# Kernel optimization log

Measured on AMD Instinct MI355X. Metric: run time of the kernel, lower is better.

The kernel has to match this reference:

```python
import jax, jax.numpy as jnp
import numpy as np

V, E, H, L, B, T = 20000, 128, 192, 3, 256, 512


def _lstm_dir(x, W_ih, W_hh, b, reverse):
    """One direction of one LSTM layer. x: [B,T,I] -> (outputs [B,T,H], final h [B,H]).
    PyTorch gate order: i, f, g, o. b = b_ih + b_hh (summed, same math)."""
    gx = jnp.einsum('bti,gi->tbg', x, W_ih) + b  # [T,B,4H] input contributions, precomputed
    Wh = W_hh.T                                   # [H,4H]

    def step(carry, g):
        h, c = carry
        z = g + h @ Wh                            # [B,4H]
        i, f, gg, o = jnp.split(z, 4, axis=-1)
        c = jax.nn.sigmoid(f) * c + jax.nn.sigmoid(i) * jnp.tanh(gg)
        h = jax.nn.sigmoid(o) * jnp.tanh(c)
        return (h, c), h

    h0 = jnp.zeros((x.shape[0], H), x.dtype)
    (hT, _), hs = jax.lax.scan(step, (h0, h0), gx, reverse=reverse)
    return hs.transpose(1, 0, 2), hT


def setup_inputs() -> dict:
    key = jax.random.key(0)
    ks = jax.random.split(key, 12)
    k = 1.0 / np.sqrt(H)
    u = lambda kk, shape: jax.random.uniform(kk, shape, jnp.float32, -k, k)
    emb = jax.random.normal(ks[0], (V, E), jnp.float32)
    emb = emb.at[0].set(0.0)  # padding_idx=0
    return {
        'x': jax.random.randint(ks[1], (B, T), 0, V),
        'emb': emb,
        'W_ih0': u(ks[2], (2, 4 * H, E)),        # layer 0, [dir, 4H, E]
        'W_hh0': u(ks[3], (2, 4 * H, H)),
        'b0': u(ks[4], (2, 4 * H)) + u(ks[5], (2, 4 * H)),  # b_ih + b_hh
        'W_ih_r': u(ks[6], (L - 1, 2, 4 * H, 2 * H)),       # layers 1..2 take concat(fwd,bwd)
        'W_hh_r': u(ks[7], (L - 1, 2, 4 * H, H)),
        'b_r': u(ks[8], (L - 1, 2, 4 * H)) + u(ks[9], (L - 1, 2, 4 * H)),
        'fc_w': u(ks[10], (1, 2 * H)),
        'fc_b': u(ks[11], (1,)),
    }


def reference(x, emb, W_ih0, W_hh0, b0, W_ih_r, W_hh_r, b_r, fc_w, fc_b):
    h = emb[x]  # [B,T,E]
    hT_f = hT_b = None
    for l in range(L):
        if l == 0:
            Wi, Wh, bb = W_ih0, W_hh0, b0
        else:
            Wi, Wh, bb = W_ih_r[l - 1], W_hh_r[l - 1], b_r[l - 1]
        out_f, hT_f = _lstm_dir(h, Wi[0], Wh[0], bb[0], reverse=False)
        out_b, hT_b = _lstm_dir(h, Wi[1], Wh[1], bb[1], reverse=True)
        h = jnp.concatenate([out_f, out_b], axis=-1)  # [B,T,2H]
        # inter-layer dropout is inactive at inference
    last = jnp.concatenate([hT_f, hT_b], axis=-1)     # [B,2H]  (hidden[-2], hidden[-1])
    return last @ fc_w.T + fc_b                        # [B,1]
```

## Files before the change

### kernel.cpp

```cpp
#include <hip/hip_runtime.h>
#include <hip/hip_bf16.h>


typedef _Float16 f16;
typedef unsigned int u32;
typedef _Float16 f16x8 __attribute__((ext_vector_type(8)));
typedef float f32x4 __attribute__((ext_vector_type(4)));

__device__ __forceinline__ float sigm(float x) {
  float e = __builtin_amdgcn_exp2f(x * -1.44269504088896f);
  return __builtin_amdgcn_rcpf(1.0f + e);
}
__device__ __forceinline__ float tanh_(float x) {
  float e = __builtin_amdgcn_exp2f(x * -2.88539008177793f);
  return __builtin_fmaf(2.0f, __builtin_amdgcn_rcpf(1.0f + e), -1.0f);
}


__global__ void castk(const float* __restrict__ s, f16* __restrict__ d, int n) {
  int i = blockIdx.x * 256 + threadIdx.x;
  int st = gridDim.x * 256;
  for (; i < n; i += st) d[i] = (f16)s[i];
}

__global__ void castwhh(const float* __restrict__ src, f16* __restrict__ dst) {
  int o = blockIdx.x * 256 + threadIdx.x;
  int e = o & 7, rest = o >> 3;
  int l = rest & 63; rest >>= 6;
  int kk = rest % 6; rest /= 6;
  int g = rest & 3; rest >>= 2;
  int w = rest % 12; int dir = rest / 12;
  int lo16 = l & 15, lhi = l >> 4;
  dst[o] = (f16)src[(size_t)(dir * 768 + g * 192 + w * 16 + lo16) * 192 + kk * 32 + lhi * 8 + e];
}

__global__ void embedk(const int* __restrict__ x, const float* __restrict__ emb,
                       f16* __restrict__ A0) {
  int row = blockIdx.x * 8 + (threadIdx.x >> 5);
  int t = row >> 8, b = row & 255;
  int xi = x[b * 512 + t];
  int c = (threadIdx.x & 31) * 4;
  float4 v = *(const float4*)(emb + (size_t)xi * 128 + c);
  union { f16 h[4]; uint2 u; } p;
  p.h[0] = (f16)v.x; p.h[1] = (f16)v.y; p.h[2] = (f16)v.z; p.h[3] = (f16)v.w;
  *(uint2*)(A0 + (size_t)row * 128 + c) = p.u;
}

template <int KD>
__global__ __launch_bounds__(768)
void fusedk(const f16* __restrict__ in, const f16* __restrict__ Bt,
            const float* __restrict__ bias,
            const u32* __restrict__ gxR, u32* __restrict__ gxW,
            const f16* __restrict__ whh16,
            f16* __restrict__ outh, float* __restrict__ hT,
            f16* __restrict__ carh, float* __restrict__ carc,
            int c, int cg, int NC, int TC, int doLstm, int wOut, int wHT) {
  union SMem {
    struct { uint4 A[512]; uint4 B[1536]; } g;
    f16 hb[2][16 * 200];
  };
  __shared__ __align__(16) SMem sm;
  const int wg = blockIdx.x;
  const int tid = threadIdx.x;
  const int l = tid & 63, w = tid >> 6;
  const int lo16 = l & 15, lhi = l >> 4;
  const int TCm1 = TC - 1;

  if (doLstm && wg < 32) {
    const int dir = wg & 1, bblk = wg >> 1;
    const int u0 = w * 16;
    const int bb = bblk * 16 + lhi * 4;
    const int dc = dir * 192;
    const int hb0 = lhi * 800 + u0 + lo16;

    f16x8 wf[4][6];
#pragma unroll
    for (int g = 0; g < 4; ++g)
#pragma unroll
      for (int kk = 0; kk < 6; ++kk)
        wf[g][kk] = *(const f16x8*)(whh16 + ((((size_t)dir * 12 + w) * 4 + g) * 6 + kk) * 512 + l * 8);

    float cq[4];
    if (c == 0) {
      f16* hz = (f16*)sm.hb;
      for (int i = tid; i < 2 * 16 * 200; i += 768) hz[i] = (f16)0.f;
#pragma unroll
      for (int q = 0; q < 4; ++q) cq[q] = 0.f;
    } else {
#pragma unroll
      for (int q = 0; q < 4; ++q) {
        size_t ci = ((size_t)dir * 256 + bb + q) * 192 + u0 + lo16;
        cq[q] = carc[ci];
        sm.hb[0][(lhi * 4 + q) * 200 + u0 + lo16] = carh[ci];
      }
    }
    __syncthreads();

    const int tb0 = dir ? (511 - c * TC) : (c * TC);
    f16* outp = outh + ((size_t)tb0 * 256 + bb) * 384 + dc + u0 + lo16;
    const ptrdiff_t ostep = dir ? -(ptrdiff_t)98304 : (ptrdiff_t)98304;

    u32 ga[8], gb[8];
    {
      const int tl0 = dir ? TCm1 : 0;
      size_t wb = ((((size_t)dir * TC + tl0) * 16 + bblk) * 12 + w) * 512;
#pragma unroll
      for (int k2 = 0; k2 < 8; ++k2) ga[k2] = gxR[wb + k2 * 64 + l];
    }

#define RSTEP(S, CUR, NXT)                                                         \
  do {                                                                             \
    {                                                                              \
      int snx = ((S) + 1 < TC) ? (S) + 1 : (S);                                    \
      int tln = dir ? (TCm1 - snx) : snx;                                          \
      size_t wb = ((((size_t)dir * TC + tln) * 16 + bblk) * 12 + w) * 512;         \
      _Pragma("unroll") for (int k2 = 0; k2 < 8; ++k2) NXT[k2] = gxR[wb + k2 * 64 + l]; \
    }                                                                              \
    f32x4 ac[4];                                                                   \
    _Pragma("unroll") for (int g_ = 0; g_ < 4; ++g_) {                             \
      union { u32 u; f16 h[2]; } p0, p1;                                           \
      p0.u = CUR[2 * g_]; p1.u = CUR[2 * g_ + 1];                                  \
      ac[g_][0] = (float)p0.h[0]; ac[g_][1] = (float)p0.h[1];                      \
      ac[g_][2] = (float)p1.h[0]; ac[g_][3] = (float)p1.h[1];                      \
    }                                                                              \
    {                                                                              \
      const f16* hcur = sm.hb[(S) & 1];                                            \
      _Pragma("unroll") for (int kk = 0; kk < 6; ++kk) {                           \
        f16x8 av = *(const f16x8*)(hcur + lo16 * 200 + kk * 32 + lhi * 8);         \
        ac[0] = __builtin_amdgcn_mfma_f32_16x16x32_f16(av, wf[0][kk], ac[0], 0, 0, 0); \
        ac[1] = __builtin_amdgcn_mfma_f32_16x16x32_f16(av, wf[1][kk], ac[1], 0, 0, 0); \
        ac[2] = __builtin_amdgcn_mfma_f32_16x16x32_f16(av, wf[2][kk], ac[2], 0, 0, 0); \
        ac[3] = __builtin_amdgcn_mfma_f32_16x16x32_f16(av, wf[3][kk], ac[3], 0, 0, 0); \
      }                                                                            \
    }                                                                              \
    f16* hnew = sm.hb[((S) + 1) & 1];                                              \
    _Pragma("unroll") for (int q = 0; q < 4; ++q) {                                \
      float iv = sigm(ac[0][q]), fv = sigm(ac[1][q]);                              \
      float gv = tanh_(ac[2][q]), ov = sigm(ac[3][q]);                             \
      cq[q] = fv * cq[q] + iv * gv;                                                \
      float hv = ov * tanh_(cq[q]);                                                \
      f16 hh = (f16)hv;                                                            \
      hnew[hb0 + q * 200] = hh;                                                    \
      if (wOut) outp[q * 384] = hh;                                                \
      if ((S) == TCm1) {                                                           \
        size_t ci = ((size_t)dir * 256 + bb + q) * 192 + u0 + lo16;                \
        carh[ci] = hh;                                                             \
        carc[ci] = cq[q];                                                          \
        if (wHT && c == NC - 1) hT[ci] = hv;                                       \
      }                                                                            \
    }                                                                              \
    outp += ostep;                                                                 \
    asm volatile("s_waitcnt lgkmcnt(0)" ::: "memory");                             \
    __builtin_amdgcn_s_barrier();                                                  \
    asm volatile("" ::: "memory");                                                 \
  } while (0)

    for (int s = 0; s < TC; s += 2) {
      RSTEP(s, ga, gb);
      RSTEP(s + 1, gb, ga);
    }
#undef RSTEP
    return;
  }

  if (cg >= NC) return;
  const int pool = doLstm ? 224 : 256;
  const int gid = doLstm ? wg - 32 : wg;
  const int RT = TC * 4;
  const int ntiles = RT * 8;
  const int tbf = cg * TC, tbb = 512 - (cg + 1) * TC;
  const int wmm = w / 6, wn = w % 6;
  constexpr int NKc = KD / 64;

  for (int tt = gid; tt < ntiles; tt += pool) {
    const int g = tt & 3;
    const int r = (tt >> 2) % RT;
    const int dir = (tt >> 2) / RT;
    const size_t ar0 = (size_t)(dir ? tbb : tbf) * 256 + r * 64;
    const int btr0 = dir * 768 + g * 192;

    float bj[2];
#pragma unroll
    for (int j = 0; j < 2; ++j) bj[j] = bias[btr0 + wn * 32 + j * 16 + lo16];

    f32x4 acc[2][2] = {};
    uint4 a0v, b0v, b1v;

#define LDG(ko_)                                                                   \
  do {                                                                             \
    if (tid < 512) {                                                               \
      int row = tid >> 3, sl = tid & 7, ch = sl ^ (row & 7);                       \
      a0v = *(const uint4*)(in + (ar0 + row) * KD + (ko_)*64 + ch * 8);            \
    }                                                                              \
    { int row = tid >> 3, sl = tid & 7, ch = sl ^ (row & 7);                       \
      b0v = *(const uint4*)(Bt + (size_t)(btr0 + row) * KD + (ko_)*64 + ch * 8); } \
    { int idx = tid + 768; int row = idx >> 3, sl = idx & 7, ch = sl ^ (row & 7);  \
      b1v = *(const uint4*)(Bt + (size_t)(btr0 + row) * KD + (ko_)*64 + ch * 8); } \
  } while (0)

    LDG(0);
    for (int ko = 0; ko < NKc; ++ko) {
      __syncthreads();
      if (tid < 512) sm.g.A[tid] = a0v;
      sm.g.B[tid] = b0v;
      sm.g.B[tid + 768] = b1v;
      __syncthreads();
      if (ko + 1 < NKc) LDG(ko + 1);
#pragma unroll
      for (int kk = 0; kk < 2; ++kk) {
        f16x8 af[2], bf[2];
#pragma unroll
        for (int i = 0; i < 2; ++i) {
          int rowA = wmm * 32 + i * 16 + lo16;
          int slA = (kk * 4 + lhi) ^ (rowA & 7);
          af[i] = *(const f16x8*)((const char*)sm.g.A + rowA * 128 + slA * 16);
        }
#pragma unroll
        for (int j = 0; j < 2; ++j) {
          int colB = wn * 32 + j * 16 + lo16;
          int slB = (kk * 4 + lhi) ^ (colB & 7);
          bf[j] = *(const f16x8*)((const char*)sm.g.B + colB * 128 + slB * 16);
        }
#pragma unroll
        for (int i = 0; i < 2; ++i)
#pragma unroll
          for (int j = 0; j < 2; ++j)
            acc[i][j] = __builtin_amdgcn_mfma_f32_16x16x32_f16(af[i], bf[j], acc[i][j], 0, 0, 0);
      }
    }
#undef LDG

#pragma unroll
    for (int i = 0; i < 2; ++i) {
      int rl = r * 64 + wmm * 32 + i * 16 + lhi * 4;
      int tl = rl >> 8;
      int b16 = (rl & 255) >> 4;
#pragma unroll
      for (int j = 0; j < 2; ++j) {
        int w12 = wn * 2 + j;
        size_t base = ((((size_t)dir * TC + tl) * 16 + b16) * 12 + w12) * 512;
#pragma unroll
        for (int qq = 0; qq < 2; ++qq) {
          union { f16 h[2]; u32 u; } p;
          p.h[0] = (f16)(acc[i][j][2 * qq] + bj[j]);
          p.h[1] = (f16)(acc[i][j][2 * qq + 1] + bj[j]);
          gxW[base + (g * 2 + qq) * 64 + l] = p.u;
        }
      }
    }
    __syncthreads();
  }
}

__global__ void fck(const float* __restrict__ hT, const float* __restrict__ w,
                    const float* __restrict__ fb, float* __restrict__ out) {
  int b = blockIdx.x * 64 + threadIdx.x;
  float a = fb[0];
#pragma unroll 4
  for (int u = 0; u < 192; ++u)
    a += w[u] * hT[(size_t)b * 192 + u] + w[192 + u] * hT[49152 + (size_t)b * 192 + u];
  out[b] = a;
}

extern "C" void kernel_launch(void* const* d_in, const int* in_sizes, int n_in,
                              void* d_out, int out_size, void* d_ws, size_t ws_size,
                              hipStream_t stream) {
  (void)in_sizes; (void)n_in; (void)out_size;
  const int* x = (const int*)d_in[0];
  const float* emb = (const float*)d_in[1];
  const float* Wih0 = (const float*)d_in[2];
  const float* Whh0 = (const float*)d_in[3];
  const float* b0 = (const float*)d_in[4];
  const float* Wihr = (const float*)d_in[5];
  const float* Whhr = (const float*)d_in[6];
  const float* br = (const float*)d_in[7];
  const float* fcw = (const float*)d_in[8];
  const float* fcb = (const float*)d_in[9];
  float* out = (float*)d_out;

  const size_t hB = 100663296ull;
  const size_t fixedB = 2 * hB + 1179648ull + 589824ull + 393216ull + 196608ull + 393216ull;

  int TC = (ws_size >= fixedB + 2ull * 16 * 786432ull) ? 16 : 8;
  const int NC = 512 / TC;
  const size_t chunkB = (size_t)TC * 786432ull;

  char* ws = (char*)d_ws;
  u32* gxb[2] = {(u32*)ws, (u32*)(ws + chunkB)};
  size_t off = 2 * chunkB;
  f16* h0 = (f16*)(ws + off); off += hB;
  f16* h1 = (f16*)(ws + off); off += hB;
  f16* A0 = h1;
  f16* Bt = (f16*)(ws + off); off += 1179648ull;
  f16* whh16 = (f16*)(ws + off); off += 589824ull;
  float* hT = (float*)(ws + off); off += 393216ull;
  f16* carh = (f16*)(ws + off); off += 196608ull;
  float* carc = (float*)(ws + off); off += 393216ull;

  embedk<<<16384, 256, 0, stream>>>(x, emb, A0);

  for (int layer = 0; layer < 3; ++layer) {
    const f16* in = (layer == 0) ? A0 : (layer == 1 ? h0 : h1);
    f16* outp = (layer == 1) ? h1 : h0;
    const int wOut = (layer < 2) ? 1 : 0;
    const int wHT = (layer == 2) ? 1 : 0;
    const float* bias = (layer == 0) ? b0 : (br + (layer - 1) * 1536);

    if (layer == 0) {
      castk<<<192, 256, 0, stream>>>(Wih0, Bt, 196608);
      castwhh<<<1152, 256, 0, stream>>>(Whh0, whh16);
    } else {
      castk<<<1152, 256, 0, stream>>>(Wihr + (size_t)(layer - 1) * 589824, Bt, 589824);
      castwhh<<<1152, 256, 0, stream>>>(Whhr + (size_t)(layer - 1) * 294912, whh16);
    }

    if (layer == 0)
      fusedk<128><<<256, 768, 0, stream>>>(in, Bt, bias, gxb[0], gxb[0], whh16,
                                           outp, hT, carh, carc, 0, 0, NC, TC, 0, wOut, wHT);
    else
      fusedk<384><<<256, 768, 0, stream>>>(in, Bt, bias, gxb[0], gxb[0], whh16,
                                           outp, hT, carh, carc, 0, 0, NC, TC, 0, wOut, wHT);

    for (int c = 0; c < NC; ++c) {
      const u32* gR = gxb[c & 1];
      u32* gW = gxb[(c + 1) & 1];
      if (layer == 0)
        fusedk<128><<<256, 768, 0, stream>>>(in, Bt, bias, gR, gW, whh16,
                                             outp, hT, carh, carc, c, c + 1, NC, TC, 1, wOut, wHT);
      else
        fusedk<384><<<256, 768, 0, stream>>>(in, Bt, bias, gR, gW, whh16,
                                             outp, hT, carh, carc, c, c + 1, NC, TC, 1, wOut, wHT);
    }
  }

  fck<<<4, 64, 0, stream>>>(hT, fcw, fcb, out);
}
```

Measured before the change: 2.779 ms.

## Replace per-chunk launches with a persistent cooperative kernel using grid syncs

```diff
diff --git a/kernel.cpp b/kernel.cpp
--- a/kernel.cpp
+++ b/kernel.cpp
@@ -1,5 +1,8 @@
 #include <hip/hip_runtime.h>
 #include <hip/hip_bf16.h>
+#include <hip/hip_cooperative_groups.h>
+
+namespace cg = cooperative_groups;
 
 
 typedef _Float16 f16;
@@ -47,26 +50,26 @@
 }
 
 template <int KD>
-__global__ __launch_bounds__(768)
-void fusedk(const f16* __restrict__ in, const f16* __restrict__ Bt,
-            const float* __restrict__ bias,
-            const u32* __restrict__ gxR, u32* __restrict__ gxW,
-            const f16* __restrict__ whh16,
-            f16* __restrict__ outh, float* __restrict__ hT,
-            f16* __restrict__ carh, float* __restrict__ carc,
-            int c, int cg, int NC, int TC, int doLstm, int wOut, int wHT) {
+__global__ __launch_bounds__(768, 3)
+void persistk(const f16* __restrict__ in, const f16* __restrict__ Bt,
+              const float* __restrict__ bias,
+              u32* __restrict__ gx0, u32* __restrict__ gx1,
+              const f16* __restrict__ whh16,
+              f16* __restrict__ outh, float* __restrict__ hT,
+              int NC, int TC, int wOut, int wHT) {
   union SMem {
     struct { uint4 A[512]; uint4 B[1536]; } g;
     f16 hb[2][16 * 200];
   };
   __shared__ __align__(16) SMem sm;
+  cg::grid_group grid = cg::this_grid();
   const int wg = blockIdx.x;
   const int tid = threadIdx.x;
   const int l = tid & 63, w = tid >> 6;
   const int lo16 = l & 15, lhi = l >> 4;
   const int TCm1 = TC - 1;
 
-  if (doLstm && wg < 32) {
+  if (wg < 32) {
     const int dir = wg & 1, bblk = wg >> 1;
     const int u0 = w * 16;
     const int bb = bblk * 16 + lhi * 4;
@@ -80,33 +83,29 @@
       for (int kk = 0; kk < 6; ++kk)
         wf[g][kk] = *(const f16x8*)(whh16 + ((((size_t)dir * 12 + w) * 4 + g) * 6 + kk) * 512 + l * 8);
 
-    float cq[4];
-    if (c == 0) {
+    {
       f16* hz = (f16*)sm.hb;
       for (int i = tid; i < 2 * 16 * 200; i += 768) hz[i] = (f16)0.f;
-#pragma unroll
-      for (int q = 0; q < 4; ++q) cq[q] = 0.f;
-    } else {
-#pragma unroll
-      for (int q = 0; q < 4; ++q) {
-        size_t ci = ((size_t)dir * 256 + bb + q) * 192 + u0 + lo16;
-        cq[q] = carc[ci];
-        sm.hb[0][(lhi * 4 + q) * 200 + u0 + lo16] = carh[ci];
-      }
     }
     __syncthreads();
-
-    const int tb0 = dir ? (511 - c * TC) : (c * TC);
-    f16* outp = outh + ((size_t)tb0 * 256 + bb) * 384 + dc + u0 + lo16;
+    float cq[4] = {0.f, 0.f, 0.f, 0.f};
+
+    f16* outp = outh + ((size_t)(dir ? 511 : 0) * 256 + bb) * 384 + dc + u0 + lo16;
     const ptrdiff_t ostep = dir ? -(ptrdiff_t)98304 : (ptrdiff_t)98304;
 
+    grid.sync();
+    __builtin_amdgcn_fence(__ATOMIC_ACQUIRE, "agent");
+
     u32 ga[8], gb[8];
-    {
-      const int tl0 = dir ? TCm1 : 0;
-      size_t wb = ((((size_t)dir * TC + tl0) * 16 + bblk) * 12 + w) * 512;
-#pragma unroll
-      for (int k2 = 0; k2 < 8; ++k2) ga[k2] = gxR[wb + k2 * 64 + l];
-    }
+    for (int c = 0; c < NC; ++c) {
+      const u32* __restrict__ gxR = (c & 1) ? gx1 : gx0;
+      const int lastc = (wHT && c == NC - 1) ? 1 : 0;
+      {
+        const int tl0 = dir ? TCm1 : 0;
+        size_t wb = ((((size_t)dir * TC + tl0) * 16 + bblk) * 12 + w) * 512;
+#pragma unroll
+        for (int k2 = 0; k2 < 8; ++k2) ga[k2] = gxR[wb + k2 * 64 + l];
+      }
 
 #define RSTEP(S, CUR, NXT)                                                         \
   do {                                                                             \
@@ -142,12 +141,8 @@
       f16 hh = (f16)hv;                                                            \
       hnew[hb0 + q * 200] = hh;                                                    \
       if (wOut) outp[q * 384] = hh;                                                \
-      if ((S) == TCm1) {                                                           \
-        size_t ci = ((size_t)dir * 256 + bb + q) * 192 + u0 + lo16;                \
-        carh[ci] = hh;                                                             \
-        carc[ci] = cq[q];                                                          \
-        if (wHT && c == NC - 1) hT[ci] = hv;                                       \
-      }                                                                            \
+      if (lastc && (S) == TCm1)                                                    \
+        hT[((size_t)dir * 256 + bb + q) * 192 + u0 + lo16] = hv;                   \
     }                                                                              \
     outp += ostep;                                                                 \
     asm volatile("s_waitcnt lgkmcnt(0)" ::: "memory");                             \
@@ -155,36 +150,40 @@
     asm volatile("" ::: "memory");                                                 \
   } while (0)
 
-    for (int s = 0; s < TC; s += 2) {
-      RSTEP(s, ga, gb);
-      RSTEP(s + 1, gb, ga);
+      for (int s = 0; s < TC; s += 2) {
+        RSTEP(s, ga, gb);
+        RSTEP(s + 1, gb, ga);
+      }
+#undef RSTEP
+      grid.sync();
+      __builtin_amdgcn_fence(__ATOMIC_ACQUIRE, "agent");
     }
-#undef RSTEP
     return;
   }
 
-  if (cg >= NC) return;
-  const int pool = doLstm ? 224 : 256;
-  const int gid = doLstm ? wg - 32 : wg;
+  const int gid = wg - 32;
   const int RT = TC * 4;
   const int ntiles = RT * 8;
-  const int tbf = cg * TC, tbb = 512 - (cg + 1) * TC;
   const int wmm = w / 6, wn = w % 6;
   constexpr int NKc = KD / 64;
 
-  for (int tt = gid; tt < ntiles; tt += pool) {
-    const int g = tt & 3;
-    const int r = (tt >> 2) % RT;
-    const int dir = (tt >> 2) / RT;
-    const size_t ar0 = (size_t)(dir ? tbb : tbf) * 256 + r * 64;
-    const int btr0 = dir * 768 + g * 192;
-
-    float bj[2];
-#pragma unroll
-    for (int j = 0; j < 2; ++j) bj[j] = bias[btr0 + wn * 32 + j * 16 + lo16];
-
-    f32x4 acc[2][2] = {};
-    uint4 a0v, b0v, b1v;
+  for (int c = 0; c < NC; ++c) {
+    u32* __restrict__ gxW = (c & 1) ? gx1 : gx0;
+    const int tbf = c * TC, tbb = 512 - (c + 1) * TC;
+
+    for (int tt = gid; tt < ntiles; tt += 224) {
+      const int g = tt & 3;
+      const int r = (tt >> 2) % RT;
+      const int dir = (tt >> 2) / RT;
+      const size_t ar0 = (size_t)(dir ? tbb : tbf) * 256 + r * 64;
+      const int btr0 = dir * 768 + g * 192;
+
+      float bj[2];
+#pragma unroll
+      for (int j = 0; j < 2; ++j) bj[j] = bias[btr0 + wn * 32 + j * 16 + lo16];
+
+      f32x4 acc[2][2] = {};
+      uint4 a0v, b0v, b1v;
 
 #define LDG(ko_)                                                                   \
   do {                                                                             \
@@ -198,58 +197,61 @@
       b1v = *(const uint4*)(Bt + (size_t)(btr0 + row) * KD + (ko_)*64 + ch * 8); } \
   } while (0)
 
-    LDG(0);
-    for (int ko = 0; ko < NKc; ++ko) {
-      __syncthreads();
-      if (tid < 512) sm.g.A[tid] = a0v;
-      sm.g.B[tid] = b0v;
-      sm.g.B[tid + 768] = b1v;
-      __syncthreads();
-      if (ko + 1 < NKc) LDG(ko + 1);
-#pragma unroll
-      for (int kk = 0; kk < 2; ++kk) {
-        f16x8 af[2], bf[2];
-#pragma unroll
-        for (int i = 0; i < 2; ++i) {
-          int rowA = wmm * 32 + i * 16 + lo16;
-          int slA = (kk * 4 + lhi) ^ (rowA & 7);
-          af[i] = *(const f16x8*)((const char*)sm.g.A + rowA * 128 + slA * 16);
-        }
-#pragma unroll
-        for (int j = 0; j < 2; ++j) {
-          int colB = wn * 32 + j * 16 + lo16;
-          int slB = (kk * 4 + lhi) ^ (colB & 7);
-          bf[j] = *(const f16x8*)((const char*)sm.g.B + colB * 128 + slB * 16);
-        }
-#pragma unroll
-        for (int i = 0; i < 2; ++i)
-#pragma unroll
-          for (int j = 0; j < 2; ++j)
-            acc[i][j] = __builtin_amdgcn_mfma_f32_16x16x32_f16(af[i], bf[j], acc[i][j], 0, 0, 0);
-      }
-    }
-#undef LDG
-
-#pragma unroll
-    for (int i = 0; i < 2; ++i) {
-      int rl = r * 64 + wmm * 32 + i * 16 + lhi * 4;
-      int tl = rl >> 8;
-      int b16 = (rl & 255) >> 4;
-#pragma unroll
-      for (int j = 0; j < 2; ++j) {
-        int w12 = wn * 2 + j;
-        size_t base = ((((size_t)dir * TC + tl) * 16 + b16) * 12 + w12) * 512;
-#pragma unroll
-        for (int qq = 0; qq < 2; ++qq) {
-          union { f16 h[2]; u32 u; } p;
-          p.h[0] = (f16)(acc[i][j][2 * qq] + bj[j]);
-          p.h[1] = (f16)(acc[i][j][2 * qq + 1] + bj[j]);
-          gxW[base + (g * 2 + qq) * 64 + l] = p.u;
+      LDG(0);
+      for (int ko = 0; ko < NKc; ++ko) {
+        __syncthreads();
+        if (tid < 512) sm.g.A[tid] = a0v;
+        sm.g.B[tid] = b0v;
+        sm.g.B[tid + 768] = b1v;
+        __syncthreads();
+        if (ko + 1 < NKc) LDG(ko + 1);
+#pragma unroll
+        for (int kk = 0; kk < 2; ++kk) {
+          f16x8 af[2], bf[2];
+#pragma unroll
+          for (int i = 0; i < 2; ++i) {
+            int rowA = wmm * 32 + i * 16 + lo16;
+            int slA = (kk * 4 + lhi) ^ (rowA & 7);
+            af[i] = *(const f16x8*)((const char*)sm.g.A + rowA * 128 + slA * 16);
+          }
+#pragma unroll
+          for (int j = 0; j < 2; ++j) {
+            int colB = wn * 32 + j * 16 + lo16;
+            int slB = (kk * 4 + lhi) ^ (colB & 7);
+            bf[j] = *(const f16x8*)((const char*)sm.g.B + colB * 128 + slB * 16);
+          }
+#pragma unroll
+          for (int i = 0; i < 2; ++i)
+#pragma unroll
+            for (int j = 0; j < 2; ++j)
+              acc[i][j] = __builtin_amdgcn_mfma_f32_16x16x32_f16(af[i], bf[j], acc[i][j], 0, 0, 0);
         }
       }
+#undef LDG
+
+#pragma unroll
+      for (int i = 0; i < 2; ++i) {
+        int rl = r * 64 + wmm * 32 + i * 16 + lhi * 4;
+        int tl = rl >> 8;
+        int b16 = (rl & 255) >> 4;
+#pragma unroll
+        for (int j = 0; j < 2; ++j) {
+          int w12 = wn * 2 + j;
+          size_t base = ((((size_t)dir * TC + tl) * 16 + b16) * 12 + w12) * 512;
+#pragma unroll
+          for (int qq = 0; qq < 2; ++qq) {
+            union { f16 h[2]; u32 u; } p;
+            p.h[0] = (f16)(acc[i][j][2 * qq] + bj[j]);
+            p.h[1] = (f16)(acc[i][j][2 * qq + 1] + bj[j]);
+            gxW[base + (g * 2 + qq) * 64 + l] = p.u;
+          }
+        }
+      }
+      __syncthreads();
     }
-    __syncthreads();
+    grid.sync();
   }
+  grid.sync();
 }
 
 __global__ void fck(const float* __restrict__ hT, const float* __restrict__ w,
@@ -279,33 +281,26 @@
   float* out = (float*)d_out;
 
   const size_t hB = 100663296ull;
-  const size_t fixedB = 2 * hB + 1179648ull + 589824ull + 393216ull + 196608ull + 393216ull;
+  const size_t fixedB = 2 * hB + 1179648ull + 589824ull + 393216ull;
 
   int TC = (ws_size >= fixedB + 2ull * 16 * 786432ull) ? 16 : 8;
   const int NC = 512 / TC;
   const size_t chunkB = (size_t)TC * 786432ull;
 
   char* ws = (char*)d_ws;
-  u32* gxb[2] = {(u32*)ws, (u32*)(ws + chunkB)};
+  u32* gx0 = (u32*)ws;
+  u32* gx1 = (u32*)(ws + chunkB);
   size_t off = 2 * chunkB;
   f16* h0 = (f16*)(ws + off); off += hB;
   f16* h1 = (f16*)(ws + off); off += hB;
   f16* A0 = h1;
   f16* Bt = (f16*)(ws + off); off += 1179648ull;
   f16* whh16 = (f16*)(ws + off); off += 589824ull;
-  float* hT = (float*)(ws + off); off += 393216ull;
-  f16* carh = (f16*)(ws + off); off += 196608ull;
-  float* carc = (float*)(ws + off); off += 393216ull;
+  float* hTp = (float*)(ws + off); off += 393216ull;
 
   embedk<<<16384, 256, 0, stream>>>(x, emb, A0);
 
   for (int layer = 0; layer < 3; ++layer) {
-    const f16* in = (layer == 0) ? A0 : (layer == 1 ? h0 : h1);
-    f16* outp = (layer == 1) ? h1 : h0;
-    const int wOut = (layer < 2) ? 1 : 0;
-    const int wHT = (layer == 2) ? 1 : 0;
-    const float* bias = (layer == 0) ? b0 : (br + (layer - 1) * 1536);
-
     if (layer == 0) {
       castk<<<192, 256, 0, stream>>>(Wih0, Bt, 196608);
       castwhh<<<1152, 256, 0, stream>>>(Whh0, whh16);
@@ -314,24 +309,24 @@
       castwhh<<<1152, 256, 0, stream>>>(Whhr + (size_t)(layer - 1) * 294912, whh16);
     }
 
+    const f16* a_in = (layer == 0) ? A0 : (layer == 1 ? h0 : h1);
+    const f16* a_bt = Bt;
+    const float* a_bias = (layer == 0) ? b0 : (br + (layer - 1) * 1536);
+    u32* a_g0 = gx0;
+    u32* a_g1 = gx1;
+    const f16* a_whh = whh16;
+    f16* a_out = (layer == 1) ? h1 : h0;
+    float* a_ht = hTp;
+    int a_nc = NC, a_tc = TC;
+    int a_wout = (layer < 2) ? 1 : 0;
+    int a_wht = (layer == 2) ? 1 : 0;
+    void* ka[12] = {&a_in, &a_bt, &a_bias, &a_g0, &a_g1, &a_whh,
+                    &a_out, &a_ht, &a_nc, &a_tc, &a_wout, &a_wht};
     if (layer == 0)
-      fusedk<128><<<256, 768, 0, stream>>>(in, Bt, bias, gxb[0], gxb[0], whh16,
-                                           outp, hT, carh, carc, 0, 0, NC, TC, 0, wOut, wHT);
+      hipLaunchCooperativeKernel(persistk<128>, dim3(256), dim3(768), ka, 0u, stream);
     else
-      fusedk<384><<<256, 768, 0, stream>>>(in, Bt, bias, gxb[0], gxb[0], whh16,
-                                           outp, hT, carh, carc, 0, 0, NC, TC, 0, wOut, wHT);
-
-    for (int c = 0; c < NC; ++c) {
-      const u32* gR = gxb[c & 1];
-      u32* gW = gxb[(c + 1) & 1];
-      if (layer == 0)
-        fusedk<128><<<256, 768, 0, stream>>>(in, Bt, bias, gR, gW, whh16,
-                                             outp, hT, carh, carc, c, c + 1, NC, TC, 1, wOut, wHT);
-      else
-        fusedk<384><<<256, 768, 0, stream>>>(in, Bt, bias, gR, gW, whh16,
-                                             outp, hT, carh, carc, c, c + 1, NC, TC, 1, wOut, wHT);
-    }
+      hipLaunchCooperativeKernel(persistk<384>, dim3(256), dim3(768), ka, 0u, stream);
   }
 
-  fck<<<4, 64, 0, stream>>>(hT, fcw, fcb, out);
-}
+  fck<<<4, 64, 0, stream>>>(hTp, fcw, fcb, out);
+}
```

New measurement: 5.335 ms. 92.0% more time.
